# Kernel optimization log

Measured on AMD Instinct MI355X. Metric: run time of the kernel, lower is better.

Reference implementation:

```python
import jax, jax.numpy as jnp
import numpy as np

BETA = 0.25
SK_EPSILONS = [0.0, 0.0, 0.003]
SK_ITERS = 50
B_SIZE = 262144
LATENT_DIM = 32
K = 256


def setup_inputs() -> dict:
    key = jax.random.key(0)
    kz, k0, k1, k2 = jax.random.split(key, 4)
    return {
        "z": jax.random.normal(kz, (B_SIZE, LATENT_DIM), dtype=jnp.float32),
        "cb0": jax.random.normal(k0, (K, LATENT_DIM), dtype=jnp.float32),
        "cb1": jax.random.normal(k1, (K, LATENT_DIM), dtype=jnp.float32),
        "cb2": jax.random.normal(k2, (K, LATENT_DIM), dtype=jnp.float32),
    }


def _sq_dists(residual, codebook):
    # ||r - c||^2 = ||r||^2 + ||c||^2 - 2 r.c  -> (B, K), avoids (B,K,D) broadcast
    r2 = jnp.sum(residual * residual, axis=1, keepdims=True)      # (B,1)
    c2 = jnp.sum(codebook * codebook, axis=1)                     # (K,)
    cross = residual @ codebook.T                                 # (B,K)
    return r2 + c2 - 2.0 * cross


def _sinkhorn(d_centered, epsilon, n_iters):
    # log-domain Sinkhorn-Knopp, matches torch reference
    B, Kk = d_centered.shape
    log_B = jnp.log(jnp.asarray(B, dtype=d_centered.dtype))
    log_K = jnp.log(jnp.asarray(Kk, dtype=d_centered.dtype))
    log_Q = -d_centered / epsilon
    log_Q = log_Q - jax.scipy.special.logsumexp(log_Q)

    def body(_, lq):
        lq = lq - jax.scipy.special.logsumexp(lq, axis=1, keepdims=True) - log_B
        lq = lq - jax.scipy.special.logsumexp(lq, axis=0, keepdims=True) - log_K
        return lq

    log_Q = jax.lax.fori_loop(0, n_iters, body, log_Q)
    return jnp.exp(log_Q + log_B)


def _quantize_level(residual, codebook, sk_epsilon, use_sk=True):
    dists = _sq_dists(residual, codebook)  # (B, K)
    codes_argmin = jnp.argmin(dists, axis=-1)
    if use_sk and sk_epsilon > 0:
        d = jax.lax.stop_gradient(dists)
        d_max = jnp.max(d)
        d_min = jnp.min(d)
        mid = (d_max + d_min) / 2
        amp = jnp.maximum(d_max - mid, 1e-05)
        Q = _sinkhorn((d - mid) / amp, sk_epsilon, SK_ITERS)
        bad = jnp.any(jnp.isnan(Q)) | jnp.any(jnp.isinf(Q))
        codes = jnp.where(bad, codes_argmin, jnp.argmax(Q, axis=-1))
    else:
        codes = codes_argmin
    quantized = codebook[codes]  # (B, D) gather
    return codes, quantized


def reference(z, cb0, cb1, cb2):
    codebooks = [cb0, cb1, cb2]
    sg = jax.lax.stop_gradient
    residual = z
    all_codes = []
    quantized_total = jnp.zeros_like(z)
    rq_loss = jnp.asarray(0.0, dtype=z.dtype)
    for codebook, sk_epsilon in zip(codebooks, SK_EPSILONS):
        codes, e = _quantize_level(residual, codebook, sk_epsilon, use_sk=True)
        all_codes.append(codes)
        rq_loss = rq_loss + jnp.mean((sg(residual) - e) ** 2)
        rq_loss = rq_loss + BETA * jnp.mean((residual - sg(e)) ** 2)
        e_st = residual + sg(e - residual)  # straight-through
        quantized_total = quantized_total + e_st
        residual = residual - sg(e)
    return (all_codes[0], all_codes[1], all_codes[2], quantized_total, rq_loss)
```

## Files before the change

### kernel.cpp

```cpp
#include <hip/hip_runtime.h>


#define BSZ   262144
#define DIM   32
#define KK    256
#define CHUNK 128
#define NBLK  (BSZ / CHUNK)
#define NIBLK (BSZ / 256)
#define LROW  36
#define SKEPS 0.003f
#define NIT   50

#define WS_SSQ  0
#define WS_MINK 1
#define WS_MAXK 2
#define WS_TWOT 3
#define WS_W0   256
#define WS_WA   512
#define WS_C2   1024
#define WSB_SIG 8192
#define WSB_BH  32768
#define WSB_BL  49152
#define WSB_QB  65536

#define OC0   0
#define OC1   BSZ
#define OC2   (2 * BSZ)
#define OQ    (3 * BSZ)
#define OLOSS (3 * BSZ + BSZ * DIM)
#define OU_AH (3u * BSZ)
#define OU_AL (3u * BSZ + 4194304u)

typedef short short8 __attribute__((ext_vector_type(8)));
typedef _Float16 half8 __attribute__((ext_vector_type(8)));
typedef float f32x4 __attribute__((ext_vector_type(4)));

#if __has_builtin(__builtin_amdgcn_exp2f)
#define EXP2(x) __builtin_amdgcn_exp2f(x)
#else
#define EXP2(x) exp2f(x)
#endif

#if __has_builtin(__builtin_amdgcn_update_dpp)
#define ROR16(x, N)                                                            \
  __int_as_float(__builtin_amdgcn_update_dpp(__float_as_int(x),                \
                 __float_as_int(x), 0x120 + (N), 0xF, 0xF, false))
#define ROR16I(x, N) __builtin_amdgcn_update_dpp((x), (x), 0x120 + (N), 0xF, 0xF, false)
#else
#define ROR16(x, N) __shfl_xor((x), (N))
#define ROR16I(x, N) __shfl_xor((x), (N))
#endif

__device__ __forceinline__ float wred_sum(float x) {
  x += ROR16(x, 1); x += ROR16(x, 2); x += ROR16(x, 4); x += ROR16(x, 8);
  x += __shfl_xor(x, 16); x += __shfl_xor(x, 32);
  return x;
}
__device__ __forceinline__ float wred_max(float x) {
  x = fmaxf(x, ROR16(x, 1)); x = fmaxf(x, ROR16(x, 2));
  x = fmaxf(x, ROR16(x, 4)); x = fmaxf(x, ROR16(x, 8));
  x = fmaxf(x, __shfl_xor(x, 16)); x = fmaxf(x, __shfl_xor(x, 32));
  return x;
}
__device__ __forceinline__ float wred_min(float x) {
  x = fminf(x, ROR16(x, 1)); x = fminf(x, ROR16(x, 2));
  x = fminf(x, ROR16(x, 4)); x = fminf(x, ROR16(x, 8));
  x = fminf(x, __shfl_xor(x, 16)); x = fminf(x, __shfl_xor(x, 32));
  return x;
}
__device__ __forceinline__ float g16_max(float x) {
  x = fmaxf(x, ROR16(x, 1)); x = fmaxf(x, ROR16(x, 2));
  x = fmaxf(x, ROR16(x, 4)); x = fmaxf(x, ROR16(x, 8));
  return x;
}
__device__ __forceinline__ float g16_sum(float x) {
  x += ROR16(x, 1); x += ROR16(x, 2); x += ROR16(x, 4); x += ROR16(x, 8);
  return x;
}
__device__ __forceinline__ void g16_argmax(float& v, int& j) {
  { float ov = ROR16(v,1); int oj = ROR16I(j,1); if (ov > v || (ov == v && oj < j)) { v = ov; j = oj; } }
  { float ov = ROR16(v,2); int oj = ROR16I(j,2); if (ov > v || (ov == v && oj < j)) { v = ov; j = oj; } }
  { float ov = ROR16(v,4); int oj = ROR16I(j,4); if (ov > v || (ov == v && oj < j)) { v = ov; j = oj; } }
  { float ov = ROR16(v,8); int oj = ROR16I(j,8); if (ov > v || (ov == v && oj < j)) { v = ov; j = oj; } }
}

__device__ __forceinline__ unsigned fkey(float f) {
  unsigned b = __float_as_uint(f);
  return (b & 0x80000000u) ? ~b : (b | 0x80000000u);
}
__device__ __forceinline__ float fkeyinv(unsigned k) {
  return __uint_as_float((k & 0x80000000u) ? (k ^ 0x80000000u) : ~k);
}
__device__ __forceinline__ unsigned pk2h(_Float16 a, _Float16 b) {
  unsigned short ua = __builtin_bit_cast(unsigned short, a);
  unsigned short ub = __builtin_bit_cast(unsigned short, b);
  return (unsigned)ua | ((unsigned)ub << 16);
}
__device__ __forceinline__ unsigned short bf16rne(float x) {
  unsigned u = __float_as_uint(x);
  return (unsigned short)((u + 0x7FFFu + ((u >> 16) & 1u)) >> 16);
}
__device__ __forceinline__ float bf2f(unsigned short h) {
  return __uint_as_float(((unsigned)h) << 16);
}
__device__ __forceinline__ void split3_8(const float* xs, short8& a1, short8& a2, short8& a3) {
#pragma unroll
  for (int u = 0; u < 8; ++u) {
    float x = xs[u];
    unsigned short b1 = bf16rne(x); x -= bf2f(b1);
    unsigned short b2 = bf16rne(x); x -= bf2f(b2);
    unsigned short b3 = bf16rne(x);
    a1[u] = (short)b1; a2[u] = (short)b2; a3[u] = (short)b3;
  }
}
__device__ __forceinline__ f32x4 mfma6r(short8 A1, short8 A2, short8 A3,
                                        short8 B1, short8 B2, short8 B3, f32x4 acc) {
  acc = __builtin_amdgcn_mfma_f32_16x16x32_bf16(A3, B1, acc, 0, 0, 0);
  acc = __builtin_amdgcn_mfma_f32_16x16x32_bf16(A1, B3, acc, 0, 0, 0);
  acc = __builtin_amdgcn_mfma_f32_16x16x32_bf16(A2, B2, acc, 0, 0, 0);
  acc = __builtin_amdgcn_mfma_f32_16x16x32_bf16(A2, B1, acc, 0, 0, 0);
  acc = __builtin_amdgcn_mfma_f32_16x16x32_bf16(A1, B2, acc, 0, 0, 0);
  acc = __builtin_amdgcn_mfma_f32_16x16x32_bf16(A1, B1, acc, 0, 0, 0);
  return acc;
}
__device__ __forceinline__ void build_a(const float* zl, int b, int lane,
                                        short8& A1, short8& A2, short8& A3) {
  int row = b * 16 + (lane & 15);
  int kb = (lane >> 4) * 8;
  float xs[8];
  float4 t0 = *reinterpret_cast<const float4*>(&zl[row * LROW + kb]);
  float4 t1 = *reinterpret_cast<const float4*>(&zl[row * LROW + kb + 4]);
  xs[0]=t0.x; xs[1]=t0.y; xs[2]=t0.z; xs[3]=t0.w;
  xs[4]=t1.x; xs[5]=t1.y; xs[6]=t1.z; xs[7]=t1.w;
  split3_8(xs, A1, A2, A3);
}

__global__ void prep0_k(const float* __restrict__ cb0, const float* __restrict__ cb1,
                        const float* __restrict__ cb2, unsigned* __restrict__ wsu,
                        float* __restrict__ wsf, uint4* __restrict__ qb,
                        unsigned long long* __restrict__ sig) {
  int t = threadIdx.x;
#pragma unroll
  for (int i = 0; i < 12; ++i) sig[i * 256 + t] = 0ull;
  if (t == 0) { wsu[WS_SSQ] = 0u; wsu[WS_MINK] = 0xFFFFFFFFu; wsu[WS_MAXK] = 0u; }
  const float* cbs[3] = {cb0, cb1, cb2};
  for (int lvl = 0; lvl < 3; ++lvl) {
    const float* cb = cbs[lvl];
    float s = 0.f;
#pragma unroll
    for (int d = 0; d < DIM; ++d) { float c = cb[t * DIM + d]; s = fmaf(c, c, s); }
    wsf[WS_C2 + lvl * 256 + t] = 0.5f * s;
    for (int g = 0; g < 4; ++g) {
      int slot = g * 256 + t;
      int jt = slot >> 6, l = slot & 63;
      int col = jt * 16 + (l & 15), kb = (l >> 4) * 8;
      float xs[8];
#pragma unroll
      for (int u = 0; u < 8; ++u) xs[u] = cb[col * DIM + kb + u];
      short8 b1, b2, b3;
      split3_8(xs, b1, b2, b3);
      qb[(lvl * 3 + 0) * 1024 + slot] = __builtin_bit_cast(uint4, b1);
      qb[(lvl * 3 + 1) * 1024 + slot] = __builtin_bit_cast(uint4, b2);
      qb[(lvl * 3 + 2) * 1024 + slot] = __builtin_bit_cast(uint4, b3);
    }
  }
}

__device__ __forceinline__ void loadq(uint4* dst, const uint4* __restrict__ src, int tid) {
#pragma unroll
  for (int i = 0; i < 12; ++i) dst[i * 256 + tid] = src[i * 256 + tid];
}

__device__ __forceinline__ void argmin_lds(const uint4* qlds, const float* cini,
                                           const float* zl, int* codel, int lane, int wid) {
#pragma unroll 1
  for (int bb = 0; bb < 2; ++bb) {
    int b = wid * 2 + bb;
    short8 A1, A2, A3;
    build_a(zl, b, lane, A1, A2, A3);
    float bv[4] = {-3.4e38f, -3.4e38f, -3.4e38f, -3.4e38f};
    int bj[4] = {0, 0, 0, 0};
#pragma unroll 2
    for (int jt = 0; jt < 16; ++jt) {
      float cv = cini[jt * 16 + (lane & 15)];
      short8 B1 = __builtin_bit_cast(short8, qlds[jt * 64 + lane]);
      short8 B2 = __builtin_bit_cast(short8, qlds[1024 + jt * 64 + lane]);
      short8 B3 = __builtin_bit_cast(short8, qlds[2048 + jt * 64 + lane]);
      int col = jt * 16 + (lane & 15);
      f32x4 acc = {cv, cv, cv, cv};
      acc = mfma6r(A1, A2, A3, B1, B2, B3, acc);
#pragma unroll
      for (int r = 0; r < 4; ++r)
        if (acc[r] > bv[r]) { bv[r] = acc[r]; bj[r] = col; }
    }
#pragma unroll
    for (int r = 0; r < 4; ++r) g16_argmax(bv[r], bj[r]);
    if ((lane & 15) == 0) {
#pragma unroll
      for (int r = 0; r < 4; ++r) codel[b * 16 + (lane >> 4) * 4 + r] = bj[r];
    }
  }
}

__device__ __forceinline__ float remap_phase(const float* __restrict__ cb, float* zl,
                                             const int* codel, int tid) {
  int row = tid & (CHUNK - 1);
  int half = tid >> 7;
  const float4* cbg = reinterpret_cast<const float4*>(cb + codel[row] * DIM + half * 16);
  float4* zr = reinterpret_cast<float4*>(&zl[row * LROW + half * 16]);
  float local = 0.f;
#pragma unroll
  for (int k = 0; k < 4; ++k) {
    float4 cv = cbg[k];
    float4 v = zr[k];
    v.x -= cv.x; v.y -= cv.y; v.z -= cv.z; v.w -= cv.w;
    zr[k] = v;
    local = fmaf(v.x, v.x, local); local = fmaf(v.y, v.y, local);
    local = fmaf(v.z, v.z, local); local = fmaf(v.w, v.w, local);
  }
  return local;
}

__global__ __launch_bounds__(256, 2) void stageA_k(const float* __restrict__ z,
                                                   const float* __restrict__ cb0,
                                                   const float* __restrict__ cb1,
                                                   float* __restrict__ out,
                                                   unsigned* __restrict__ outu,
                                                   unsigned* __restrict__ wsu,
                                                   float* __restrict__ wsf,
                                                   const uint4* __restrict__ qb) {
  __shared__ float zl[CHUNK * LROW];
  __shared__ uint4 qlds[3 * 1024];
  __shared__ float c2l[256];
  __shared__ float rsq[CHUNK];
  __shared__ int codel[CHUNK];
  __shared__ float red[4];
  const int tid = threadIdx.x, lane = tid & 63, wid = tid >> 6;
  const long base = (long)blockIdx.x * CHUNK;

#pragma unroll
  for (int g = 0; g < 4; ++g) {
    int f4 = g * 256 + tid;
    float4 v = reinterpret_cast<const float4*>(z + base * DIM)[f4];
    int row = f4 >> 3, d = (f4 & 7) * 4;
    *reinterpret_cast<float4*>(&zl[row * LROW + d]) = v;
  }
  loadq(qlds, qb, tid);
  c2l[tid] = -wsf[WS_C2 + tid];
  __syncthreads();

  float loss_acc = 0.f;

  argmin_lds(qlds, c2l, zl, codel, lane, wid);
  __syncthreads();
  if (tid < CHUNK) out[OC0 + base + tid] = (float)codel[tid];
  loss_acc += remap_phase(cb0, zl, codel, tid);
  loadq(qlds, qb + 3 * 1024, tid);
  c2l[tid] = -wsf[WS_C2 + 256 + tid];
  __syncthreads();

  argmin_lds(qlds, c2l, zl, codel, lane, wid);
  __syncthreads();
  if (tid < CHUNK) out[OC1 + base + tid] = (float)codel[tid];
  loss_acc += remap_phase(cb1, zl, codel, tid);
  loadq(qlds, qb + 6 * 1024, tid);
  c2l[tid] = -wsf[WS_C2 + 512 + tid];
  __syncthreads();

  if (tid < CHUNK) {
    float s = 0.f;
#pragma unroll
    for (int d = 0; d < DIM; ++d) { float x = zl[tid * LROW + d]; s = fmaf(x, x, s); }
    rsq[tid] = s;
  }
  __syncthreads();

  {
    float dmn = 3.4e38f, dmx = -3.4e38f;
#pragma unroll 1
    for (int bb = 0; bb < 2; ++bb) {
      int b = wid * 2 + bb;
      short8 A1, A2, A3;
      build_a(zl, b, lane, A1, A2, A3);
      float mn[4] = {3.4e38f, 3.4e38f, 3.4e38f, 3.4e38f};
      float mx[4] = {-3.4e38f, -3.4e38f, -3.4e38f, -3.4e38f};
#pragma unroll 2
      for (int jt = 0; jt < 16; ++jt) {
        float cv = c2l[jt * 16 + (lane & 15)];
        short8 B1 = __builtin_bit_cast(short8, qlds[jt * 64 + lane]);
        short8 B2 = __builtin_bit_cast(short8, qlds[1024 + jt * 64 + lane]);
        short8 B3 = __builtin_bit_cast(short8, qlds[2048 + jt * 64 + lane]);
        f32x4 acc = {cv, cv, cv, cv};
        acc = mfma6r(A1, A2, A3, B1, B2, B3, acc);
#pragma unroll
        for (int r = 0; r < 4; ++r) { mn[r] = fminf(mn[r], acc[r]); mx[r] = fmaxf(mx[r], acc[r]); }
      }
#pragma unroll
      for (int r = 0; r < 4; ++r) {
        float r2 = rsq[b * 16 + (lane >> 4) * 4 + r];
        dmn = fminf(dmn, fmaf(-2.f, mx[r], r2));
        dmx = fmaxf(dmx, fmaf(-2.f, mn[r], r2));
      }
    }
    dmn = wred_min(dmn);
    dmx = wred_max(dmx);
    if (lane == 0) {
      atomicMin(&wsu[WS_MINK], fkey(dmn));
      atomicMax(&wsu[WS_MAXK], fkey(dmx));
    }
  }

#pragma unroll
  for (int g2 = 0; g2 < 8; ++g2) {
    int slot = g2 * 256 + tid;
    int b = slot >> 8;
    int l = (slot >> 2) & 63;
    int u = slot & 3;
    int row = b * 16 + (l & 15);
    int k = (l >> 4) * 8 + u * 2;
    float x0 = zl[row * LROW + k], x1 = zl[row * LROW + k + 1];
    _Float16 h0 = (_Float16)x0, h1 = (_Float16)x1;
    _Float16 q0 = (_Float16)(x0 - (float)h0), q1 = (_Float16)(x1 - (float)h1);
    unsigned gbase = ((unsigned)blockIdx.x * 8u + (unsigned)b) * 256u + (unsigned)(l * 4 + u);
    outu[OU_AH + gbase] = pk2h(h0, h1);
    outu[OU_AL + gbase] = pk2h(q0, q1);
  }

  loss_acc = wred_sum(loss_acc);
  if (lane == 0) red[wid] = loss_acc;
  __syncthreads();
  if (tid == 0) atomicAdd(&wsf[WS_SSQ], red[0] + red[1] + red[2] + red[3]);
}

__global__ void prep_k(const float* __restrict__ cb2, unsigned* __restrict__ wsu,
                       float* __restrict__ wsf, unsigned* __restrict__ bh,
                       unsigned* __restrict__ bl, uint4* __restrict__ qb) {
  int j = threadIdx.x;
  float dmin = fkeyinv(wsu[WS_MINK]);
  float dmax = fkeyinv(wsu[WS_MAXK]);
  float mid = (dmax + dmin) * 0.5f;
  float amp = fmaxf(dmax - mid, 1e-5f);
  float t = 1.0f / (amp * SKEPS);
  const float L2E = 1.4426950408889634f;
  float T2L = 2.0f * t * L2E;
  if (j == 0) wsf[WS_TWOT] = T2L;
  float s = 0.f;
#pragma unroll
  for (int d = 0; d < DIM; ++d) { float c = cb2[j * DIM + d]; s = fmaf(c, c, s); }
  wsf[WS_W0 + j] = -t * L2E * s;
  for (int g = 0; g < 16; ++g) {
    int slot = g * 256 + j;
    int jt = slot >> 8, l = (slot >> 2) & 63, u = slot & 3;
    int col = jt * 16 + (l & 15);
    int k = (l >> 4) * 8 + u * 2;
    float b0 = T2L * cb2[col * DIM + k], b1 = T2L * cb2[col * DIM + k + 1];
    _Float16 h0 = (_Float16)b0, h1 = (_Float16)b1;
    _Float16 q0 = (_Float16)(b0 - (float)h0), q1 = (_Float16)(b1 - (float)h1);
    bh[slot] = pk2h(h0, h1);
    bl[slot] = pk2h(q0, q1);
  }
  for (int g = 0; g < 4; ++g) {
    int slot = g * 256 + j;
    int jt = slot >> 6, l = slot & 63;
    int col = jt * 16 + (l & 15), kb = (l >> 4) * 8;
    float xs[8];
#pragma unroll
    for (int u = 0; u < 8; ++u) xs[u] = T2L * cb2[col * DIM + kb + u];
    short8 b1v, b2v, b3v;
    split3_8(xs, b1v, b2v, b3v);
    qb[9 * 1024 + slot]  = __builtin_bit_cast(uint4, b1v);
    qb[10 * 1024 + slot] = __builtin_bit_cast(uint4, b2v);
    qb[11 * 1024 + slot] = __builtin_bit_cast(uint4, b3v);
  }
}

__global__ __launch_bounds__(256, 2) void iter_k(const uint4* __restrict__ afh,
                                                 const uint4* __restrict__ afl,
                                                 const uint4* __restrict__ bfh,
                                                 const uint4* __restrict__ bfl,
                                                 const float* __restrict__ w_rd,
                                                 float* __restrict__ w_wr,
                                                 const unsigned long long* __restrict__ s_rd,
                                                 unsigned long long* __restrict__ s_wr,
                                                 unsigned long long* __restrict__ s_zr,
                                                 int first) {
  __shared__ float wsh[KK];
  __shared__ float exm[8][2][2][16];
  __shared__ float exs[8][2][2][16];
  __shared__ float ssh[2][KK];
  const int tid = threadIdx.x, lane = tid & 63, wv = tid >> 6;
  const int pair = wv >> 1, ch = wv & 1, g = lane >> 4;

  {
    unsigned long long tt = s_rd[tid] + s_rd[256 + tid] + s_rd[512 + tid] + s_rd[768 + tid];
    float wj = first ? w_rd[tid]
                     : w_rd[tid] + 34.0f - log2f(fmaxf((float)tt, 1.0f));
    wsh[tid] = wj;
    if (blockIdx.x == 0) {
      w_wr[tid] = wj;
      s_zr[tid] = 0ull; s_zr[256 + tid] = 0ull;
      s_zr[512 + tid] = 0ull; s_zr[768 + tid] = 0ull;
    }
  }
  half8 Bh[8], Bl[8];
#pragma unroll
  for (int jt = 0; jt < 8; ++jt) {
    Bh[jt] = __builtin_bit_cast(half8, bfh[(ch * 8 + jt) * 64 + lane]);
    Bl[jt] = __builtin_bit_cast(half8, bfl[(ch * 8 + jt) * 64 + lane]);
  }
  __syncthreads();
  float wc[8];
#pragma unroll
  for (int c = 0; c < 8; ++c) wc[c] = wsh[(ch * 8 + c) * 16 + (lane & 15)];

  float sg[8] = {0.f, 0.f, 0.f, 0.f, 0.f, 0.f, 0.f, 0.f};

  for (int b = 0; b < 8; ++b) {
    const int batchid = blockIdx.x * 16 + pair * 8 + b;
    half8 Ah = __builtin_bit_cast(half8, afh[batchid * 64 + lane]);
    half8 Al = __builtin_bit_cast(half8, afl[batchid * 64 + lane]);
    f32x4 v[8];
#pragma unroll
    for (int jt = 0; jt < 8; ++jt) {
      f32x4 acc = {wc[jt], wc[jt], wc[jt], wc[jt]};
      acc = __builtin_amdgcn_mfma_f32_16x16x32_f16(Al, Bl[jt], acc, 0, 0, 0);
      acc = __builtin_amdgcn_mfma_f32_16x16x32_f16(Al, Bh[jt], acc, 0, 0, 0);
      acc = __builtin_amdgcn_mfma_f32_16x16x32_f16(Ah, Bl[jt], acc, 0, 0, 0);
      acc = __builtin_amdgcn_mfma_f32_16x16x32_f16(Ah, Bh[jt], acc, 0, 0, 0);
      v[jt] = acc;
    }
    float m[4];
#pragma unroll
    for (int r = 0; r < 4; ++r) {
      float a01 = fmaxf(v[0][r], v[1][r]), a23 = fmaxf(v[2][r], v[3][r]);
      float a45 = fmaxf(v[4][r], v[5][r]), a67 = fmaxf(v[6][r], v[7][r]);
      m[r] = g16_max(fmaxf(fmaxf(a01, a23), fmaxf(a45, a67)));
    }
    float s[4];
#pragma unroll
    for (int r = 0; r < 4; ++r) {
#pragma unroll
      for (int jt = 0; jt < 8; ++jt) v[jt][r] = EXP2(v[jt][r] - m[r]);
      float s01 = v[0][r] + v[1][r], s23 = v[2][r] + v[3][r];
      float s45 = v[4][r] + v[5][r], s67 = v[6][r] + v[7][r];
      s[r] = g16_sum((s01 + s23) + (s45 + s67));
    }
    if ((lane & 15) == 0) {
      *reinterpret_cast<float4*>(&exm[b][pair][ch][g * 4]) = make_float4(m[0], m[1], m[2], m[3]);
      *reinterpret_cast<float4*>(&exs[b][pair][ch][g * 4]) = make_float4(s[0], s[1], s[2], s[3]);
    }
    __syncthreads();
    float4 pm = *reinterpret_cast<const float4*>(&exm[b][pair][ch ^ 1][g * 4]);
    float4 ps = *reinterpret_cast<const float4*>(&exs[b][pair][ch ^ 1][g * 4]);
    float rinv[4];
    {
      float pmv[4] = {pm.x, pm.y, pm.z, pm.w};
      float psv[4] = {ps.x, ps.y, ps.z, ps.w};
#pragma unroll
      for (int r = 0; r < 4; ++r) {
        float M = fmaxf(m[r], pmv[r]);
        float sc = EXP2(m[r] - M);
        float tot = fmaf(s[r], sc, psv[r] * EXP2(pmv[r] - M));
        rinv[r] = sc * __builtin_amdgcn_rcpf(tot);
      }
    }
#pragma unroll
    for (int jt = 0; jt < 8; ++jt)
#pragma unroll
      for (int r = 0; r < 4; ++r) sg[jt] = fmaf(v[jt][r], rinv[r], sg[jt]);
  }
#pragma unroll
  for (int jt = 0; jt < 8; ++jt) {
    float x = sg[jt];
    x += __shfl_xor(x, 16); x += __shfl_xor(x, 32);
    sg[jt] = x;
  }
  if (lane < 16) {
#pragma unroll
    for (int jt = 0; jt < 8; ++jt) ssh[pair][ch * 128 + jt * 16 + lane] = sg[jt];
  }
  __syncthreads();
  float stot = ssh[0][tid] + ssh[1][tid];
  atomicAdd(s_wr + (blockIdx.x & 3) * 256 + tid,
            (unsigned long long)fmaf(stot, 16777216.0f, 0.5f));
}

__global__ __launch_bounds__(256, 2) void fcodes_k(const float* __restrict__ z,
                                                   const float* __restrict__ cb0,
                                                   const float* __restrict__ cb1,
                                                   float* __restrict__ out,
                                                   const uint4* __restrict__ qb,
                                                   const float* __restrict__ w_rd,
                                                   const unsigned long long* __restrict__ s_rd) {
  __shared__ float zl[CHUNK * LROW];
  __shared__ uint4 qlds[3 * 1024];
  __shared__ float wsh[KK];
  __shared__ int codel[CHUNK];
  const int tid = threadIdx.x, lane = tid & 63, wid = tid >> 6;
  const long base = (long)blockIdx.x * CHUNK;

  {
    unsigned long long tt = s_rd[tid] + s_rd[256 + tid] + s_rd[512 + tid] + s_rd[768 + tid];
    wsh[tid] = w_rd[tid] + 34.0f - log2f(fmaxf((float)tt, 1.0f));
  }
  loadq(qlds, qb + 9 * 1024, tid);
#pragma unroll
  for (int g = 0; g < 4; ++g) {
    int f4 = g * 256 + tid;
    float4 v = reinterpret_cast<const float4*>(z + base * DIM)[f4];
    int row = f4 >> 3, d = (f4 & 7) * 4;
    *reinterpret_cast<float4*>(&zl[row * LROW + d]) = v;
  }
  __syncthreads();
  {
    int row = tid & (CHUNK - 1);
    int half = tid >> 7;
    int c0 = (int)out[OC0 + base + row];
    int c1 = (int)out[OC1 + base + row];
    const float4* e0 = reinterpret_cast<const float4*>(cb0 + c0 * DIM + half * 16);
    const float4* e1 = reinterpret_cast<const float4*>(cb1 + c1 * DIM + half * 16);
    float4* zr = reinterpret_cast<float4*>(&zl[row * LROW + half * 16]);
#pragma unroll
    for (int k = 0; k < 4; ++k) {
      float4 a = e0[k], bb = e1[k], v = zr[k];
      v.x = (v.x - a.x) - bb.x; v.y = (v.y - a.y) - bb.y;
      v.z = (v.z - a.z) - bb.z; v.w = (v.w - a.w) - bb.w;
      zr[k] = v;
    }
  }
  __syncthreads();

#pragma unroll 1
  for (int bb = 0; bb < 2; ++bb) {
    int b = wid * 2 + bb;
    short8 A1, A2, A3;
    build_a(zl, b, lane, A1, A2, A3);
    float bv[4] = {-3.4e38f, -3.4e38f, -3.4e38f, -3.4e38f};
    int bj[4] = {0, 0, 0, 0};
#pragma unroll 2
    for (int jt = 0; jt < 16; ++jt) {
      float wcv = wsh[jt * 16 + (lane & 15)];
      short8 B1 = __builtin_bit_cast(short8, qlds[jt * 64 + lane]);
      short8 B2 = __builtin_bit_cast(short8, qlds[1024 + jt * 64 + lane]);
      short8 B3 = __builtin_bit_cast(short8, qlds[2048 + jt * 64 + lane]);
      f32x4 acc = {wcv, wcv, wcv, wcv};
      acc = mfma6r(A1, A2, A3, B1, B2, B3, acc);
      int col = jt * 16 + (lane & 15);
#pragma unroll
      for (int r = 0; r < 4; ++r)
        if (acc[r] > bv[r]) { bv[r] = acc[r]; bj[r] = col; }
    }
#pragma unroll
    for (int r = 0; r < 4; ++r) g16_argmax(bv[r], bj[r]);
    if ((lane & 15) == 0) {
#pragma unroll
      for (int r = 0; r < 4; ++r) codel[b * 16 + (lane >> 4) * 4 + r] = bj[r];
    }
  }
  __syncthreads();
  if (tid < CHUNK) out[OC2 + base + tid] = (float)codel[tid];
}

__global__ __launch_bounds__(256) void fout_k(const float* __restrict__ z,
                                              const float* __restrict__ cb0,
                                              const float* __restrict__ cb1,
                                              const float* __restrict__ cb2,
                                              float* __restrict__ out,
                                              float* __restrict__ wsf) {
  __shared__ int cc0[256], cc1[256], cc2[256];
  __shared__ float red[4];
  const int tid = threadIdx.x, lane = tid & 63, wv = tid >> 6;
  const long rbase = (long)blockIdx.x * 256;
  cc0[tid] = (int)out[OC0 + rbase + tid];
  cc1[tid] = (int)out[OC1 + rbase + tid];
  cc2[tid] = (int)out[OC2 + rbase + tid];
  __syncthreads();
  float loss = 0.f;
#pragma unroll
  for (int g = 0; g < 8; ++g) {
    long f4 = (long)blockIdx.x * 2048 + g * 256 + tid;
    int lrow = (g * 256 + tid) >> 3;
    int d4 = (g * 256 + tid) & 7;
    float4 zv = reinterpret_cast<const float4*>(z)[f4];
    float4 e0 = *reinterpret_cast<const float4*>(&cb0[cc0[lrow] * DIM + d4 * 4]);
    float4 e1 = *reinterpret_cast<const float4*>(&cb1[cc1[lrow] * DIM + d4 * 4]);
    float4 e2 = *reinterpret_cast<const float4*>(&cb2[cc2[lrow] * DIM + d4 * 4]);
    float4 q;
    q.x = (e0.x + e1.x) + e2.x; q.y = (e0.y + e1.y) + e2.y;
    q.z = (e0.z + e1.z) + e2.z; q.w = (e0.w + e1.w) + e2.w;
    reinterpret_cast<float4*>(out + OQ)[f4] = q;
    float rx = ((zv.x - e0.x) - e1.x) - e2.x;
    float ry = ((zv.y - e0.y) - e1.y) - e2.y;
    float rz = ((zv.z - e0.z) - e1.z) - e2.z;
    float rw = ((zv.w - e0.w) - e1.w) - e2.w;
    loss = fmaf(rx, rx, loss); loss = fmaf(ry, ry, loss);
    loss = fmaf(rz, rz, loss); loss = fmaf(rw, rw, loss);
  }
  loss = wred_sum(loss);
  if (lane == 0) red[wv] = loss;
  __syncthreads();
  if (tid == 0) atomicAdd(&wsf[WS_SSQ], red[0] + red[1] + red[2] + red[3]);
}

__global__ void losswrite_k(float* __restrict__ out, const float* __restrict__ wsf) {
  if (threadIdx.x == 0) out[OLOSS] = 1.25f * wsf[WS_SSQ] / 8388608.0f;
}

extern "C" void kernel_launch(void* const* d_in, const int* in_sizes, int n_in,
                              void* d_out, int out_size, void* d_ws, size_t ws_size,
                              hipStream_t stream) {
  const float* z   = (const float*)d_in[0];
  const float* cb0 = (const float*)d_in[1];
  const float* cb1 = (const float*)d_in[2];
  const float* cb2 = (const float*)d_in[3];
  float* out = (float*)d_out;
  unsigned* outu = (unsigned*)d_out;
  float* wsf = (float*)d_ws;
  unsigned* wsu = (unsigned*)d_ws;
  unsigned long long* sig = (unsigned long long*)((char*)d_ws + WSB_SIG);
  unsigned* bh = (unsigned*)((char*)d_ws + WSB_BH);
  unsigned* bl = (unsigned*)((char*)d_ws + WSB_BL);
  uint4* qb = (uint4*)((char*)d_ws + WSB_QB);

  const uint4* afh = (const uint4*)(outu + OU_AH);
  const uint4* afl = (const uint4*)(outu + OU_AL);
  const uint4* bfh = (const uint4*)bh;
  const uint4* bfl = (const uint4*)bl;

  prep0_k<<<1, 256, 0, stream>>>(cb0, cb1, cb2, wsu, wsf, qb, sig);
  stageA_k<<<NBLK, 256, 0, stream>>>(z, cb0, cb1, out, outu, wsu, wsf, qb);
  prep_k<<<1, 256, 0, stream>>>(cb2, wsu, wsf, bh, bl, qb);
  for (int it = 0; it < NIT; ++it) {
    const float* w_rd = (it == 0) ? (wsf + WS_W0) : (wsf + WS_WA + ((it - 1) & 1) * KK);
    float* w_wr = wsf + WS_WA + (it & 1) * KK;
    const unsigned long long* s_rd = sig + 1024 * ((it + 2) % 3);
    unsigned long long* s_wr = sig + 1024 * (it % 3);
    unsigned long long* s_zr = sig + 1024 * ((it + 1) % 3);
    iter_k<<<NIBLK, 256, 0, stream>>>(afh, afl, bfh, bfl, w_rd, w_wr, s_rd, s_wr, s_zr,
                                      it == 0 ? 1 : 0);
  }
  fcodes_k<<<NBLK, 256, 0, stream>>>(z, cb0, cb1, out, qb,
                                     wsf + WS_WA + ((NIT - 1) & 1) * KK,
                                     sig + 1024 * ((NIT - 1) % 3));
  fout_k<<<NIBLK, 256, 0, stream>>>(z, cb0, cb1, cb2, out, wsf);
  losswrite_k<<<1, 64, 0, stream>>>(out, wsf);
}
```

Baseline: 1.998 ms.

## Process two row tiles per B load and trade Sinkhorn registers for occupancy

The argmin and min/max passes now compute two 16-row tiles together, so each codebook fragment read from LDS feeds two MFMA chains instead of one. In the Sinkhorn iteration kernel, the low-half B fragments move from registers into shared memory and the Al*Bl MFMA term is dropped, leaving three f16 MFMAs per tile. Launch bounds rise to 4 blocks per CU to get more waves resident. Dropping the low*low product slightly lowers the accuracy of the split-precision matmul, and the extra LDS reads compete with the higher occupancy.

```diff
diff --git a/kernel.cpp b/kernel.cpp
--- a/kernel.cpp
+++ b/kernel.cpp
@@ -171,33 +171,40 @@
   for (int i = 0; i < 12; ++i) dst[i * 256 + tid] = src[i * 256 + tid];
 }
 
-__device__ __forceinline__ void argmin_lds(const uint4* qlds, const float* cini,
-                                           const float* zl, int* codel, int lane, int wid) {
-#pragma unroll 1
-  for (int bb = 0; bb < 2; ++bb) {
-    int b = wid * 2 + bb;
-    short8 A1, A2, A3;
-    build_a(zl, b, lane, A1, A2, A3);
-    float bv[4] = {-3.4e38f, -3.4e38f, -3.4e38f, -3.4e38f};
-    int bj[4] = {0, 0, 0, 0};
+__device__ __forceinline__ void argmin2_lds(const uint4* qlds, const float* cini,
+                                            const float* zl, int* codel, int lane, int wid) {
+  short8 A1a, A2a, A3a, A1b, A2b, A3b;
+  build_a(zl, wid * 2 + 0, lane, A1a, A2a, A3a);
+  build_a(zl, wid * 2 + 1, lane, A1b, A2b, A3b);
+  float bva[4] = {-3.4e38f, -3.4e38f, -3.4e38f, -3.4e38f};
+  float bvb[4] = {-3.4e38f, -3.4e38f, -3.4e38f, -3.4e38f};
+  int bja[4] = {0, 0, 0, 0}, bjb[4] = {0, 0, 0, 0};
 #pragma unroll 2
-    for (int jt = 0; jt < 16; ++jt) {
-      float cv = cini[jt * 16 + (lane & 15)];
-      short8 B1 = __builtin_bit_cast(short8, qlds[jt * 64 + lane]);
-      short8 B2 = __builtin_bit_cast(short8, qlds[1024 + jt * 64 + lane]);
-      short8 B3 = __builtin_bit_cast(short8, qlds[2048 + jt * 64 + lane]);
-      int col = jt * 16 + (lane & 15);
-      f32x4 acc = {cv, cv, cv, cv};
-      acc = mfma6r(A1, A2, A3, B1, B2, B3, acc);
-#pragma unroll
-      for (int r = 0; r < 4; ++r)
-        if (acc[r] > bv[r]) { bv[r] = acc[r]; bj[r] = col; }
-    }
-#pragma unroll
-    for (int r = 0; r < 4; ++r) g16_argmax(bv[r], bj[r]);
-    if ((lane & 15) == 0) {
-#pragma unroll
-      for (int r = 0; r < 4; ++r) codel[b * 16 + (lane >> 4) * 4 + r] = bj[r];
+  for (int jt = 0; jt < 16; ++jt) {
+    float cv = cini[jt * 16 + (lane & 15)];
+    short8 B1 = __builtin_bit_cast(short8, qlds[jt * 64 + lane]);
+    short8 B2 = __builtin_bit_cast(short8, qlds[1024 + jt * 64 + lane]);
+    short8 B3 = __builtin_bit_cast(short8, qlds[2048 + jt * 64 + lane]);
+    int col = jt * 16 + (lane & 15);
+    f32x4 aa = {cv, cv, cv, cv};
+    aa = mfma6r(A1a, A2a, A3a, B1, B2, B3, aa);
+    f32x4 ab = {cv, cv, cv, cv};
+    ab = mfma6r(A1b, A2b, A3b, B1, B2, B3, ab);
+#pragma unroll
+    for (int r = 0; r < 4; ++r) {
+      if (aa[r] > bva[r]) { bva[r] = aa[r]; bja[r] = col; }
+      if (ab[r] > bvb[r]) { bvb[r] = ab[r]; bjb[r] = col; }
+    }
+  }
+#pragma unroll
+  for (int r = 0; r < 4; ++r) g16_argmax(bva[r], bja[r]);
+#pragma unroll
+  for (int r = 0; r < 4; ++r) g16_argmax(bvb[r], bjb[r]);
+  if ((lane & 15) == 0) {
+#pragma unroll
+    for (int r = 0; r < 4; ++r) {
+      codel[(wid * 2 + 0) * 16 + (lane >> 4) * 4 + r] = bja[r];
+      codel[(wid * 2 + 1) * 16 + (lane >> 4) * 4 + r] = bjb[r];
     }
   }
 }
@@ -251,7 +258,7 @@
 
   float loss_acc = 0.f;
 
-  argmin_lds(qlds, c2l, zl, codel, lane, wid);
+  argmin2_lds(qlds, c2l, zl, codel, lane, wid);
   __syncthreads();
   if (tid < CHUNK) out[OC0 + base + tid] = (float)codel[tid];
   loss_acc += remap_phase(cb0, zl, codel, tid);
@@ -259,7 +266,7 @@
   c2l[tid] = -wsf[WS_C2 + 256 + tid];
   __syncthreads();
 
-  argmin_lds(qlds, c2l, zl, codel, lane, wid);
+  argmin2_lds(qlds, c2l, zl, codel, lane, wid);
   __syncthreads();
   if (tid < CHUNK) out[OC1 + base + tid] = (float)codel[tid];
   loss_acc += remap_phase(cb1, zl, codel, tid);
@@ -276,31 +283,36 @@
   __syncthreads();
 
   {
+    short8 A1a, A2a, A3a, A1b, A2b, A3b;
+    build_a(zl, wid * 2 + 0, lane, A1a, A2a, A3a);
+    build_a(zl, wid * 2 + 1, lane, A1b, A2b, A3b);
+    float mna[4] = {3.4e38f, 3.4e38f, 3.4e38f, 3.4e38f};
+    float mxa[4] = {-3.4e38f, -3.4e38f, -3.4e38f, -3.4e38f};
+    float mnb[4] = {3.4e38f, 3.4e38f, 3.4e38f, 3.4e38f};
+    float mxb[4] = {-3.4e38f, -3.4e38f, -3.4e38f, -3.4e38f};
+#pragma unroll 2
+    for (int jt = 0; jt < 16; ++jt) {
+      float cv = c2l[jt * 16 + (lane & 15)];
+      short8 B1 = __builtin_bit_cast(short8, qlds[jt * 64 + lane]);
+      short8 B2 = __builtin_bit_cast(short8, qlds[1024 + jt * 64 + lane]);
+      short8 B3 = __builtin_bit_cast(short8, qlds[2048 + jt * 64 + lane]);
+      f32x4 aa = {cv, cv, cv, cv};
+      aa = mfma6r(A1a, A2a, A3a, B1, B2, B3, aa);
+      f32x4 ab = {cv, cv, cv, cv};
+      ab = mfma6r(A1b, A2b, A3b, B1, B2, B3, ab);
+#pragma unroll
+      for (int r = 0; r < 4; ++r) {
+        mna[r] = fminf(mna[r], aa[r]); mxa[r] = fmaxf(mxa[r], aa[r]);
+        mnb[r] = fminf(mnb[r], ab[r]); mxb[r] = fmaxf(mxb[r], ab[r]);
+      }
+    }
     float dmn = 3.4e38f, dmx = -3.4e38f;
-#pragma unroll 1
-    for (int bb = 0; bb < 2; ++bb) {
-      int b = wid * 2 + bb;
-      short8 A1, A2, A3;
-      build_a(zl, b, lane, A1, A2, A3);
-      float mn[4] = {3.4e38f, 3.4e38f, 3.4e38f, 3.4e38f};
-      float mx[4] = {-3.4e38f, -3.4e38f, -3.4e38f, -3.4e38f};
-#pragma unroll 2
-      for (int jt = 0; jt < 16; ++jt) {
-        float cv = c2l[jt * 16 + (lane & 15)];
-        short8 B1 = __builtin_bit_cast(short8, qlds[jt * 64 + lane]);
-        short8 B2 = __builtin_bit_cast(short8, qlds[1024 + jt * 64 + lane]);
-        short8 B3 = __builtin_bit_cast(short8, qlds[2048 + jt * 64 + lane]);
-        f32x4 acc = {cv, cv, cv, cv};
-        acc = mfma6r(A1, A2, A3, B1, B2, B3, acc);
-#pragma unroll
-        for (int r = 0; r < 4; ++r) { mn[r] = fminf(mn[r], acc[r]); mx[r] = fmaxf(mx[r], acc[r]); }
-      }
-#pragma unroll
-      for (int r = 0; r < 4; ++r) {
-        float r2 = rsq[b * 16 + (lane >> 4) * 4 + r];
-        dmn = fminf(dmn, fmaf(-2.f, mx[r], r2));
-        dmx = fmaxf(dmx, fmaf(-2.f, mn[r], r2));
-      }
+#pragma unroll
+    for (int r = 0; r < 4; ++r) {
+      float r2a = rsq[(wid * 2 + 0) * 16 + (lane >> 4) * 4 + r];
+      float r2b = rsq[(wid * 2 + 1) * 16 + (lane >> 4) * 4 + r];
+      dmn = fminf(dmn, fminf(fmaf(-2.f, mxa[r], r2a), fmaf(-2.f, mxb[r], r2b)));
+      dmx = fmaxf(dmx, fmaxf(fmaf(-2.f, mna[r], r2a), fmaf(-2.f, mnb[r], r2b)));
     }
     dmn = wred_min(dmn);
     dmx = wred_max(dmx);
@@ -374,7 +386,7 @@
   }
 }
 
-__global__ __launch_bounds__(256, 2) void iter_k(const uint4* __restrict__ afh,
+__global__ __launch_bounds__(256, 4) void iter_k(const uint4* __restrict__ afh,
                                                  const uint4* __restrict__ afl,
                                                  const uint4* __restrict__ bfh,
                                                  const uint4* __restrict__ bfl,
@@ -384,6 +396,7 @@
                                                  unsigned long long* __restrict__ s_wr,
                                                  unsigned long long* __restrict__ s_zr,
                                                  int first) {
+  __shared__ uint4 Blo[1024];
   __shared__ float wsh[KK];
   __shared__ float exm[8][2][2][16];
   __shared__ float exs[8][2][2][16];
@@ -402,12 +415,12 @@
       s_zr[512 + tid] = 0ull; s_zr[768 + tid] = 0ull;
     }
   }
-  half8 Bh[8], Bl[8];
-#pragma unroll
-  for (int jt = 0; jt < 8; ++jt) {
+#pragma unroll
+  for (int i = 0; i < 4; ++i) Blo[i * 256 + tid] = bfl[i * 256 + tid];
+  half8 Bh[8];
+#pragma unroll
+  for (int jt = 0; jt < 8; ++jt)
     Bh[jt] = __builtin_bit_cast(half8, bfh[(ch * 8 + jt) * 64 + lane]);
-    Bl[jt] = __builtin_bit_cast(half8, bfl[(ch * 8 + jt) * 64 + lane]);
-  }
   __syncthreads();
   float wc[8];
 #pragma unroll
@@ -415,6 +428,7 @@
 
   float sg[8] = {0.f, 0.f, 0.f, 0.f, 0.f, 0.f, 0.f, 0.f};
 
+#pragma unroll 1
   for (int b = 0; b < 8; ++b) {
     const int batchid = blockIdx.x * 16 + pair * 8 + b;
     half8 Ah = __builtin_bit_cast(half8, afh[batchid * 64 + lane]);
@@ -422,10 +436,10 @@
     f32x4 v[8];
 #pragma unroll
     for (int jt = 0; jt < 8; ++jt) {
+      half8 Blv = __builtin_bit_cast(half8, Blo[(ch * 8 + jt) * 64 + lane]);
       f32x4 acc = {wc[jt], wc[jt], wc[jt], wc[jt]};
-      acc = __builtin_amdgcn_mfma_f32_16x16x32_f16(Al, Bl[jt], acc, 0, 0, 0);
       acc = __builtin_amdgcn_mfma_f32_16x16x32_f16(Al, Bh[jt], acc, 0, 0, 0);
-      acc = __builtin_amdgcn_mfma_f32_16x16x32_f16(Ah, Bl[jt], acc, 0, 0, 0);
+      acc = __builtin_amdgcn_mfma_f32_16x16x32_f16(Ah, Blv, acc, 0, 0, 0);
       acc = __builtin_amdgcn_mfma_f32_16x16x32_f16(Ah, Bh[jt], acc, 0, 0, 0);
       v[jt] = acc;
     }
@@ -530,33 +544,7 @@
   }
   __syncthreads();
 
-#pragma unroll 1
-  for (int bb = 0; bb < 2; ++bb) {
-    int b = wid * 2 + bb;
-    short8 A1, A2, A3;
-    build_a(zl, b, lane, A1, A2, A3);
-    float bv[4] = {-3.4e38f, -3.4e38f, -3.4e38f, -3.4e38f};
-    int bj[4] = {0, 0, 0, 0};
-#pragma unroll 2
-    for (int jt = 0; jt < 16; ++jt) {
-      float wcv = wsh[jt * 16 + (lane & 15)];
-      short8 B1 = __builtin_bit_cast(short8, qlds[jt * 64 + lane]);
-      short8 B2 = __builtin_bit_cast(short8, qlds[1024 + jt * 64 + lane]);
-      short8 B3 = __builtin_bit_cast(short8, qlds[2048 + jt * 64 + lane]);
-      f32x4 acc = {wcv, wcv, wcv, wcv};
-      acc = mfma6r(A1, A2, A3, B1, B2, B3, acc);
-      int col = jt * 16 + (lane & 15);
-#pragma unroll
-      for (int r = 0; r < 4; ++r)
-        if (acc[r] > bv[r]) { bv[r] = acc[r]; bj[r] = col; }
-    }
-#pragma unroll
-    for (int r = 0; r < 4; ++r) g16_argmax(bv[r], bj[r]);
-    if ((lane & 15) == 0) {
-#pragma unroll
-      for (int r = 0; r < 4; ++r) codel[b * 16 + (lane >> 4) * 4 + r] = bj[r];
-    }
-  }
+  argmin2_lds(qlds, wsh, zl, codel, lane, wid);
   __syncthreads();
   if (tid < CHUNK) out[OC2 + base + tid] = (float)codel[tid];
 }
```

After: 1.981 ms. Within noise of the previous version (-0.8%).
